# Performance work log

Hardware: AMD Instinct MI355X
Metric: run time of the kernel (lower is better)

Reference implementation:

```python
import jax, jax.numpy as jnp
import numpy as np

EPS = 1e-5

def _bn(x, g, b, axes):
    # BatchNorm (training-mode batch statistics), channel axis = 1
    m = jnp.mean(x, axis=axes, keepdims=True)
    v = jnp.var(x, axis=axes, keepdims=True)
    sh = [1] * x.ndim
    sh[1] = -1
    return (x - m) * jax.lax.rsqrt(v + EPS) * g.reshape(sh) + b.reshape(sh)

def _gelu(x):
    return jax.nn.gelu(x, approximate=False)  # torch nn.GELU default (erf)

def _knn_idx(x, k):
    # x: (B, C, N). Negative squared pairwise distance, take k nearest.
    inner = jnp.einsum('bcn,bcm->bnm', x, x)
    sq = jnp.sum(x * x, axis=1)                       # (B, N)
    negd = 2.0 * inner - sq[:, :, None] - sq[:, None, :]
    _, idx = jax.lax.top_k(negd, k)                   # (B, N, k) int32
    return idx

def _graph_feature(x, k):
    # x: (B, C, N) -> (B, 2C, N, k): concat(neighbor - center, center)
    idx = _knn_idx(x, k)
    xt = jnp.transpose(x, (0, 2, 1))                  # (B, N, C)
    nbr = jax.vmap(lambda xb, ib: xb[ib])(xt, idx)    # (B, N, k, C) gather
    ctr = jnp.broadcast_to(xt[:, :, None, :], nbr.shape)
    f = jnp.concatenate([nbr - ctr, ctr], axis=-1)    # (B, N, k, 2C)
    return jnp.transpose(f, (0, 3, 1, 2))             # (B, 2C, N, k)

def _edge_block(x, W, g, b, k):
    # gather -> 1x1 conv -> BN -> GELU -> max over neighbors
    f = _graph_feature(x, k)
    h = jnp.einsum('oi,bink->bonk', W, f)
    h = _gelu(_bn(h, g, b, (0, 2, 3)))
    return jnp.max(h, axis=-1)                        # (B, O, N)


def setup_inputs() -> dict:
    key = jax.random.key(0)
    ks = jax.random.split(key, 16)
    B, C, N, k = 8, 3, 1024, 20
    c = 64
    def w(kk, o, i):
        return jax.random.normal(kk, (o, i), jnp.float32) * (1.0 / np.sqrt(i))
    inp = {
        'x': jax.random.normal(ks[0], (B, C, N), jnp.float32),
        'k': k,
        'W1': w(ks[1], c, 2 * C),            # (64, 6)
        'g1': jnp.ones((c,)), 'b1': jnp.zeros((c,)),
        'W2': w(ks[2], 2 * c, 2 * c),        # (128, 128)
        'g2': jnp.ones((2 * c,)), 'b2': jnp.zeros((2 * c,)),
        'W3': w(ks[3], 4 * c, 4 * c),        # (256, 256)
        'g3': jnp.ones((4 * c,)), 'b3': jnp.zeros((4 * c,)),
        'W4': w(ks[4], 8 * c, 8 * c),        # (512, 512)
        'g4': jnp.ones((8 * c,)), 'b4': jnp.zeros((8 * c,)),
        'W5': w(ks[5], 16 * c, 15 * c),      # (1024, 960) cat(64+128+256+512)
        'g5': jnp.ones((16 * c,)), 'b5': jnp.zeros((16 * c,)),
        'Wl1': w(ks[6], 8 * c, 32 * c),      # (512, 2048), bias=False
        'g6': jnp.ones((8 * c,)), 'b6': jnp.zeros((8 * c,)),
        'Wl2': w(ks[7], 256, 512), 'bl2': jnp.zeros((256,)),
        'g7': jnp.ones((256,)), 'b7': jnp.zeros((256,)),
        'Wl3': w(ks[8], 40, 256), 'bl3': jnp.zeros((40,)),
    }
    return inp


def reference(x, k, W1, g1, b1, W2, g2, b2, W3, g3, b3, W4, g4, b4,
              W5, g5, b5, Wl1, g6, b6, Wl2, bl2, g7, b7, Wl3, bl3):
    x1 = _edge_block(x,  W1, g1, b1, k)   # (B, 64,  N)
    x2 = _edge_block(x1, W2, g2, b2, k)   # (B, 128, N)
    x3 = _edge_block(x2, W3, g3, b3, k)   # (B, 256, N)
    x4 = _edge_block(x3, W4, g4, b4, k)   # (B, 512, N)
    xc = jnp.concatenate([x1, x2, x3, x4], axis=1)  # (B, 960, N)
    h = jnp.einsum('oi,bin->bon', W5, xc)           # (B, 1024, N)
    h = _gelu(_bn(h, g5, b5, (0, 2)))
    mx = jnp.max(h, axis=-1)
    av = jnp.mean(h, axis=-1)
    z = jnp.concatenate([mx, av], axis=1)           # (B, 2048)
    z = z @ Wl1.T                                   # (B, 512), no bias
    z = jax.nn.leaky_relu(_bn(z, g6, b6, (0,)), 0.2)
    z = z @ Wl2.T + bl2                             # (B, 256)
    z = jax.nn.leaky_relu(_bn(z, g7, b7, (0,)), 0.2)
    out = z @ Wl3.T + bl3                           # (B, 40)
    return out
```

## Files before the change

kernel.cpp:

```cpp
#include <hip/hip_runtime.h>
#include <math.h>

#define BB 8
#define NN 1024
#define KNN 20

typedef unsigned short u16;
typedef __bf16 bf16x8 __attribute__((ext_vector_type(8)));
typedef float floatx4 __attribute__((ext_vector_type(4)));

__device__ __forceinline__ float gelu_erf(float x) {
    return 0.5f * x * (1.0f + erff(x * 0.70710678118654752440f));
}

__device__ __forceinline__ u16 f2bf(float f) {
    unsigned int u = __float_as_uint(f);
    unsigned int r = (u + 0x7fffu + ((u >> 16) & 1u)) >> 16;
    return (u16)r;
}
__device__ __forceinline__ float bf2f(u16 h) {
    return __uint_as_float(((unsigned int)h) << 16);
}

#define STATS_BLK 32768
#define STATS_TOTAL (4 * STATS_BLK + 16384)
#define ZERO_TOTAL (STATS_TOTAL + 3 * 8192)

__global__ void k_transpose(const float* __restrict__ x, float* __restrict__ x0,
                            float* __restrict__ sz) {
    int t = blockIdx.x * 256 + threadIdx.x;
    for (int i = t; i < ZERO_TOTAL; i += BB * NN) sz[i] = 0.f;
    if (t >= BB * NN) return;
    int b = t / NN, n = t % NN;
    #pragma unroll
    for (int c = 0; c < 3; ++c) x0[(size_t)t * 3 + c] = x[((size_t)b * 3 + c) * NN + n];
}

#define SEG2 16384
#define SEG3 81920
#define SEG4 344064
#define SEGT 1327104
__global__ void k_prep_w(const float* __restrict__ W2, const float* __restrict__ W3,
                         const float* __restrict__ W4, const float* __restrict__ W5,
                         u16* __restrict__ wh, u16* __restrict__ wl) {
    int t = blockIdx.x * 256 + threadIdx.x;
    if (t >= SEGT) return;
    float v;
    if (t < SEG2) {
        int row = t >> 6, c = t & 63;
        v = (row < 128) ? W2[row * 128 + c]
                        : W2[(row - 128) * 128 + 64 + c] - W2[(row - 128) * 128 + c];
    } else if (t < SEG3) {
        int i = t - SEG2;
        int row = i >> 7, c = i & 127;
        v = (row < 256) ? W3[row * 256 + c]
                        : W3[(row - 256) * 256 + 128 + c] - W3[(row - 256) * 256 + c];
    } else if (t < SEG4) {
        int i = t - SEG3;
        int row = i >> 8, c = i & 255;
        v = (row < 512) ? W4[row * 512 + c]
                        : W4[(row - 512) * 512 + 256 + c] - W4[(row - 512) * 512 + c];
    } else {
        int i = t - SEG4;
        int row = i / 960, c = i % 960;
        v = W5[row * 960 + c];
    }
    u16 h = f2bf(v);
    wh[t] = h;
    wl[t] = f2bf(v - bf2f(h));
}

__global__ void k_negd(const float* __restrict__ X, int SA, int Kc, float* __restrict__ out) {
    int bz = blockIdx.z;
    const float* Xb = X + (size_t)bz * NN * SA;
    float* Cout = out + (size_t)bz * NN * NN;
    int m0 = blockIdx.y * 128, n0 = blockIdx.x * 128;
    __shared__ float As[16][132];
    __shared__ float Bs[16][132];
    __shared__ float sqA[128];
    __shared__ float sqB[128];
    int t = threadIdx.x;
    int tx = t & 15, ty = t >> 4;
    int r = t >> 1, kb = (t & 1) * 8;
    float acc[2][2][4][4] = {};
    float sqa = 0.f, sqb = 0.f;
    for (int k0 = 0; k0 < Kc; k0 += 16) {
        const float* srcA = Xb + (size_t)(m0 + r) * SA + k0 + kb;
        const float* srcB = Xb + (size_t)(n0 + r) * SA + k0 + kb;
        #pragma unroll
        for (int i = 0; i < 8; ++i) {
            float va = (k0 + kb + i < Kc) ? srcA[i] : 0.f;
            float vb = (k0 + kb + i < Kc) ? srcB[i] : 0.f;
            As[kb + i][r] = va;
            Bs[kb + i][r] = vb;
            sqa = fmaf(va, va, sqa);
            sqb = fmaf(vb, vb, sqb);
        }
        __syncthreads();
        #pragma unroll
        for (int kk = 0; kk < 16; ++kk) {
            float4 a0 = *(const float4*)&As[kk][ty * 4];
            float4 a1 = *(const float4*)&As[kk][64 + ty * 4];
            float4 b0 = *(const float4*)&Bs[kk][tx * 4];
            float4 b1 = *(const float4*)&Bs[kk][64 + tx * 4];
            float av[2][4] = {{a0.x, a0.y, a0.z, a0.w}, {a1.x, a1.y, a1.z, a1.w}};
            float bv[2][4] = {{b0.x, b0.y, b0.z, b0.w}, {b1.x, b1.y, b1.z, b1.w}};
            #pragma unroll
            for (int hm = 0; hm < 2; ++hm)
                #pragma unroll
                for (int hn = 0; hn < 2; ++hn)
                    #pragma unroll
                    for (int i = 0; i < 4; ++i)
                        #pragma unroll
                        for (int j = 0; j < 4; ++j)
                            acc[hm][hn][i][j] = fmaf(av[hm][i], bv[hn][j], acc[hm][hn][i][j]);
        }
        __syncthreads();
    }
    sqa += __shfl_xor(sqa, 1);
    sqb += __shfl_xor(sqb, 1);
    if ((t & 1) == 0) { sqA[r] = sqa; sqB[r] = sqb; }
    __syncthreads();
    #pragma unroll
    for (int hm = 0; hm < 2; ++hm)
        #pragma unroll
        for (int i = 0; i < 4; ++i) {
            int lrow = hm * 64 + ty * 4 + i;
            float sm = sqA[lrow];
            float* crow = Cout + (size_t)(m0 + lrow) * NN + n0;
            #pragma unroll
            for (int hn = 0; hn < 2; ++hn) {
                float4 sn = *(const float4*)&sqB[hn * 64 + tx * 4];
                float4 v;
                v.x = 2.f * acc[hm][hn][i][0] - sm - sn.x;
                v.y = 2.f * acc[hm][hn][i][1] - sm - sn.y;
                v.z = 2.f * acc[hm][hn][i][2] - sm - sn.z;
                v.w = 2.f * acc[hm][hn][i][3] - sm - sn.w;
                *(float4*)&crow[hn * 64 + tx * 4] = v;
            }
        }
}

__global__ __launch_bounds__(256) void k_mfma_comb(
    const u16* __restrict__ Ah, const u16* __restrict__ Al,
    const u16* __restrict__ Wh, const u16* __restrict__ Wl,
    const float* __restrict__ sqg,
    float* __restrict__ negdOut, float* __restrict__ uwOut,
    int K, int ldUw) {
    const int lda = 960;
    int bx = blockIdx.x, by = blockIdx.y;
    bool gram = (by < 8);
    int m0, n0, rowBase;
    const u16 *pBh, *pBl;
    size_t ldb;
    float* pC;
    if (gram) {
        int b = bx & 7;
        n0 = (bx >> 3) * 128;
        m0 = by * 128;
        rowBase = b * NN;
        pBh = Ah; pBl = Al; ldb = lda;
        pC = negdOut + (size_t)b * NN * NN;
    } else {
        m0 = bx * 128;
        n0 = (by - 8) * 128;
        rowBase = 0;
        pBh = Wh; pBl = Wl; ldb = K;
        pC = uwOut;
    }
    __shared__ u16 sAh[4 * 1024];
    __shared__ u16 sAl[4 * 1024];
    __shared__ u16 sBh[4 * 1024];
    __shared__ u16 sBl[4 * 1024];
    __shared__ float sqA[128];
    __shared__ float sqB[128];
    int t = threadIdx.x;
    int w = t >> 6, lane = t & 63;
    int wm = (w & 1) * 64, wn = (w >> 1) * 64;
    int q = lane >> 4, lm = lane & 15;
    int r = t >> 1, cb = (t & 1) * 16;
    int q0 = (t & 1) * 2;
    if (gram) {
        if (t < 128) sqA[t] = sqg[rowBase + m0 + t];
        else if (t < 256) sqB[t - 128] = sqg[rowBase + n0 + (t - 128)];
    }
    floatx4 acc[4][4];
    #pragma unroll
    for (int i = 0; i < 4; ++i)
        #pragma unroll
        for (int j = 0; j < 4; ++j) {
            floatx4 z = {0.f, 0.f, 0.f, 0.f};
            acc[i][j] = z;
        }
    for (int k0 = 0; k0 < K; k0 += 32) {
        {
            size_t oa = (size_t)(rowBase + m0 + r) * lda + k0 + cb;
            size_t ob = gram ? (size_t)(rowBase + n0 + r) * lda + k0 + cb
                             : (size_t)(n0 + r) * ldb + k0 + cb;
            float4 ah0 = *(const float4*)&Ah[oa];
            float4 ah1 = *(const float4*)&Ah[oa + 8];
            float4 al0 = *(const float4*)&Al[oa];
            float4 al1 = *(const float4*)&Al[oa + 8];
            float4 bh0 = *(const float4*)&pBh[ob];
            float4 bh1 = *(const float4*)&pBh[ob + 8];
            float4 bl0 = *(const float4*)&pBl[ob];
            float4 bl1 = *(const float4*)&pBl[ob + 8];
            *(float4*)&sAh[q0 * 1024 + r * 8] = ah0;
            *(float4*)&sAh[(q0 + 1) * 1024 + r * 8] = ah1;
            *(float4*)&sAl[q0 * 1024 + r * 8] = al0;
            *(float4*)&sAl[(q0 + 1) * 1024 + r * 8] = al1;
            *(float4*)&sBh[q0 * 1024 + r * 8] = bh0;
            *(float4*)&sBh[(q0 + 1) * 1024 + r * 8] = bh1;
            *(float4*)&sBl[q0 * 1024 + r * 8] = bl0;
            *(float4*)&sBl[(q0 + 1) * 1024 + r * 8] = bl1;
        }
        __syncthreads();
        bf16x8 ah[4], al[4], bh[4], bl[4];
        #pragma unroll
        for (int i = 0; i < 4; ++i) {
            ah[i] = *(const bf16x8*)&sAh[q * 1024 + (wm + i * 16 + lm) * 8];
            al[i] = *(const bf16x8*)&sAl[q * 1024 + (wm + i * 16 + lm) * 8];
        }
        #pragma unroll
        for (int j = 0; j < 4; ++j) {
            bh[j] = *(const bf16x8*)&sBh[q * 1024 + (wn + j * 16 + lm) * 8];
            bl[j] = *(const bf16x8*)&sBl[q * 1024 + (wn + j * 16 + lm) * 8];
        }
        #pragma unroll
        for (int i = 0; i < 4; ++i)
            #pragma unroll
            for (int j = 0; j < 4; ++j) {
                acc[i][j] = __builtin_amdgcn_mfma_f32_16x16x32_bf16(ah[i], bh[j], acc[i][j], 0, 0, 0);
                acc[i][j] = __builtin_amdgcn_mfma_f32_16x16x32_bf16(ah[i], bl[j], acc[i][j], 0, 0, 0);
                acc[i][j] = __builtin_amdgcn_mfma_f32_16x16x32_bf16(al[i], bh[j], acc[i][j], 0, 0, 0);
            }
        __syncthreads();
    }
    if (gram) {
        #pragma unroll
        for (int i = 0; i < 4; ++i)
            #pragma unroll
            for (int j = 0; j < 4; ++j) {
                int coll = wn + j * 16 + lm;
                float sn = sqB[coll];
                #pragma unroll
                for (int rr = 0; rr < 4; ++rr) {
                    int rowl = wm + i * 16 + q * 4 + rr;
                    pC[(size_t)(m0 + rowl) * NN + n0 + coll] =
                        2.f * acc[i][j][rr] - sqA[rowl] - sn;
                }
            }
    } else {
        #pragma unroll
        for (int i = 0; i < 4; ++i) {
            int rowb = m0 + wm + i * 16 + q * 4;
            #pragma unroll
            for (int j = 0; j < 4; ++j) {
                int col = n0 + wn + j * 16 + lm;
                #pragma unroll
                for (int rr = 0; rr < 4; ++rr)
                    pC[(size_t)(rowb + rr) * ldUw + col] = acc[i][j][rr];
            }
        }
    }
}

__global__ __launch_bounds__(256) void k_mfma16(
    const u16* __restrict__ Ah, const u16* __restrict__ Al, int lda,
    const u16* __restrict__ Bh, const u16* __restrict__ Bl, int ldb,
    float* __restrict__ Cout, int ldc, int K) {
    int m0 = blockIdx.y * 128, n0 = blockIdx.x * 128;
    __shared__ u16 sAh[4 * 1024];
    __shared__ u16 sAl[4 * 1024];
    __shared__ u16 sBh[4 * 1024];
    __shared__ u16 sBl[4 * 1024];
    int t = threadIdx.x;
    int w = t >> 6, lane = t & 63;
    int wm = (w & 1) * 64, wn = (w >> 1) * 64;
    int q = lane >> 4, lm = lane & 15;
    int r = t >> 1, cb = (t & 1) * 16;
    int q0 = (t & 1) * 2;
    floatx4 acc[4][4];
    #pragma unroll
    for (int i = 0; i < 4; ++i)
        #pragma unroll
        for (int j = 0; j < 4; ++j) {
            floatx4 z = {0.f, 0.f, 0.f, 0.f};
            acc[i][j] = z;
        }
    for (int k0 = 0; k0 < K; k0 += 32) {
        {
            size_t oa = (size_t)(m0 + r) * lda + k0 + cb;
            size_t ob = (size_t)(n0 + r) * ldb + k0 + cb;
            float4 ah0 = *(const float4*)&Ah[oa];
            float4 ah1 = *(const float4*)&Ah[oa + 8];
            float4 al0 = *(const float4*)&Al[oa];
            float4 al1 = *(const float4*)&Al[oa + 8];
            float4 bh0 = *(const float4*)&Bh[ob];
            float4 bh1 = *(const float4*)&Bh[ob + 8];
            float4 bl0 = *(const float4*)&Bl[ob];
            float4 bl1 = *(const float4*)&Bl[ob + 8];
            *(float4*)&sAh[q0 * 1024 + r * 8] = ah0;
            *(float4*)&sAh[(q0 + 1) * 1024 + r * 8] = ah1;
            *(float4*)&sAl[q0 * 1024 + r * 8] = al0;
            *(float4*)&sAl[(q0 + 1) * 1024 + r * 8] = al1;
            *(float4*)&sBh[q0 * 1024 + r * 8] = bh0;
            *(float4*)&sBh[(q0 + 1) * 1024 + r * 8] = bh1;
            *(float4*)&sBl[q0 * 1024 + r * 8] = bl0;
            *(float4*)&sBl[(q0 + 1) * 1024 + r * 8] = bl1;
        }
        __syncthreads();
        bf16x8 ah[4], al[4], bh[4], bl[4];
        #pragma unroll
        for (int i = 0; i < 4; ++i) {
            ah[i] = *(const bf16x8*)&sAh[q * 1024 + (wm + i * 16 + lm) * 8];
            al[i] = *(const bf16x8*)&sAl[q * 1024 + (wm + i * 16 + lm) * 8];
        }
        #pragma unroll
        for (int j = 0; j < 4; ++j) {
            bh[j] = *(const bf16x8*)&sBh[q * 1024 + (wn + j * 16 + lm) * 8];
            bl[j] = *(const bf16x8*)&sBl[q * 1024 + (wn + j * 16 + lm) * 8];
        }
        #pragma unroll
        for (int i = 0; i < 4; ++i)
            #pragma unroll
            for (int j = 0; j < 4; ++j) {
                acc[i][j] = __builtin_amdgcn_mfma_f32_16x16x32_bf16(ah[i], bh[j], acc[i][j], 0, 0, 0);
                acc[i][j] = __builtin_amdgcn_mfma_f32_16x16x32_bf16(ah[i], bl[j], acc[i][j], 0, 0, 0);
                acc[i][j] = __builtin_amdgcn_mfma_f32_16x16x32_bf16(al[i], bh[j], acc[i][j], 0, 0, 0);
            }
        __syncthreads();
    }
    #pragma unroll
    for (int i = 0; i < 4; ++i) {
        int rowb = m0 + wm + i * 16 + q * 4;
        #pragma unroll
        for (int j = 0; j < 4; ++j) {
            int col = n0 + wn + j * 16 + lm;
            #pragma unroll
            for (int rr = 0; rr < 4; ++rr)
                Cout[(size_t)(rowb + rr) * ldc + col] = acc[i][j][rr];
        }
    }
}

__global__ void k_topk(const float* __restrict__ negd, int* __restrict__ idxout) {
    int wv = threadIdx.x >> 6, lane = threadIdx.x & 63;
    int bx = blockIdx.x;
    int b = bx & 7, rg = bx >> 3;
    int rowA = b * NN + rg * 8 + wv * 2;
    int rowB = rowA + 1;
    const float* dA = negd + (size_t)rowA * NN;
    const float* dB = negd + (size_t)rowB * NN;
    float va[16], vb[16];
    #pragma unroll
    for (int j = 0; j < 16; ++j) {
        va[j] = dA[j * 64 + lane];
        vb[j] = dB[j * 64 + lane];
    }
    float lva = va[0], lvb = vb[0];
    int lca = lane, lcb = lane;
    #pragma unroll
    for (int j = 1; j < 16; ++j) {
        int c = j * 64 + lane;
        if (va[j] > lva) { lva = va[j]; lca = c; }
        if (vb[j] > lvb) { lvb = vb[j]; lcb = c; }
    }
    for (int it = 0; it < KNN; ++it) {
        float ta = lva, tb = lvb;
        #pragma unroll
        for (int s = 32; s >= 1; s >>= 1) {
            float oa = __shfl_xor(ta, s);
            float ob = __shfl_xor(tb, s);
            ta = fmaxf(ta, oa);
            tb = fmaxf(tb, ob);
        }
        unsigned long long ma = __ballot(lva == ta);
        unsigned long long mb = __ballot(lvb == tb);
        int wa = 0x7fffffff, wb = 0x7fffffff;
        while (ma) {
            int l = __ffsll((unsigned long long)ma) - 1;
            int c = __shfl(lca, l);
            wa = min(wa, c);
            ma &= ma - 1;
        }
        while (mb) {
            int l = __ffsll((unsigned long long)mb) - 1;
            int c = __shfl(lcb, l);
            wb = min(wb, c);
            mb &= mb - 1;
        }
        if (lane == 0) {
            idxout[(size_t)rowA * KNN + it] = wa;
            idxout[(size_t)rowB * KNN + it] = wb;
        }
        if ((wa & 63) == lane) {
            int jd = wa >> 6;
            #pragma unroll
            for (int j = 0; j < 16; ++j)
                if (j == jd) va[j] = -INFINITY;
            lva = -INFINITY; lca = 0x7fffffff;
            #pragma unroll
            for (int j = 0; j < 16; ++j) {
                int c = j * 64 + lane;
                if (va[j] > lva) { lva = va[j]; lca = c; }
            }
        }
        if ((wb & 63) == lane) {
            int jd = wb >> 6;
            #pragma unroll
            for (int j = 0; j < 16; ++j)
                if (j == jd) vb[j] = -INFINITY;
            lvb = -INFINITY; lcb = 0x7fffffff;
            #pragma unroll
            for (int j = 0; j < 16; ++j) {
                int c = j * 64 + lane;
                if (vb[j] > lvb) { lvb = vb[j]; lcb = c; }
            }
        }
    }
}

__global__ void k_uw1(const float* __restrict__ x0, const float* __restrict__ W1,
                      float* __restrict__ uw) {
    int t = blockIdx.x * 256 + threadIdx.x;
    if (t >= BB * NN * 128) return;
    int r = t >> 7, o = t & 127;
    float xv0 = x0[(size_t)r * 3], xv1 = x0[(size_t)r * 3 + 1], xv2 = x0[(size_t)r * 3 + 2];
    float acc;
    if (o < 64) {
        const float* wr = W1 + (size_t)o * 6;
        acc = wr[0] * xv0 + wr[1] * xv1 + wr[2] * xv2;
    } else {
        const float* wr = W1 + (size_t)(o - 64) * 6;
        acc = (wr[3] - wr[0]) * xv0 + (wr[4] - wr[1]) * xv1 + (wr[5] - wr[2]) * xv2;
    }
    uw[(size_t)t] = acc;
}

__global__ void k_gather4(const float* __restrict__ uw, const int* __restrict__ idx,
                          int O, int ctc, int R,
                          float* __restrict__ hmin, float* __restrict__ hmax,
                          float* __restrict__ s1, float* __restrict__ s2) {
    int t = threadIdx.x;
    int ct = t % ctc, rt = t / ctc;
    int rowsPer = (R * ctc) >> 8;
    int bx = blockIdx.x;
    int b = bx & 7, rg = bx >> 3;
    int row0 = b * NN + rg * R;
    int shard = bx & 15;
    int o4 = blockIdx.y * (ctc * 4) + ct * 4;
    __shared__ int sidx[16 * KNN];
    __shared__ float4 red1[256];
    __shared__ float4 red2[256];
    for (int i = t; i < R * KNN; i += 256) sidx[i] = idx[(size_t)row0 * KNN + i];
    __syncthreads();
    int twoO = 2 * O;
    const float* ubase = uw + (size_t)b * NN * twoO;
    float a1[4] = {0, 0, 0, 0}, a2[4] = {0, 0, 0, 0};
    for (int rr = rt * rowsPer; rr < (rt + 1) * rowsPer; ++rr) {
        int nrow = row0 + rr;
        float4 w4 = *(const float4*)(uw + (size_t)nrow * twoO + O + o4);
        float wv[4] = {w4.x, w4.y, w4.z, w4.w};
        float mn[4], mx[4];
        #pragma unroll
        for (int qq = 0; qq < 4; ++qq) { mn[qq] = INFINITY; mx[qq] = -INFINITY; }
        #pragma unroll 4
        for (int j = 0; j < KNN; ++j) {
            int m = sidx[rr * KNN + j];
            float4 u4 = *(const float4*)(ubase + (size_t)m * twoO + o4);
            float uv[4] = {u4.x, u4.y, u4.z, u4.w};
            #pragma unroll
            for (int qq = 0; qq < 4; ++qq) {
                float h = uv[qq] + wv[qq];
                mn[qq] = fminf(mn[qq], h);
                mx[qq] = fmaxf(mx[qq], h);
                a1[qq] += h;
                a2[qq] = fmaf(h, h, a2[qq]);
            }
        }
        *(float4*)&hmin[(size_t)nrow * O + o4] = make_float4(mn[0], mn[1], mn[2], mn[3]);
        *(float4*)&hmax[(size_t)nrow * O + o4] = make_float4(mx[0], mx[1], mx[2], mx[3]);
    }
    red1[t] = make_float4(a1[0], a1[1], a1[2], a1[3]);
    red2[t] = make_float4(a2[0], a2[1], a2[2], a2[3]);
    __syncthreads();
    if (rt == 0) {
        int rs = 256 / ctc;
        for (int rr = 1; rr < rs; ++rr) {
            float4 v1 = red1[ct + rr * ctc];
            float4 v2 = red2[ct + rr * ctc];
            a1[0] += v1.x; a1[1] += v1.y; a1[2] += v1.z; a1[3] += v1.w;
            a2[0] += v2.x; a2[1] += v2.y; a2[2] += v2.z; a2[3] += v2.w;
        }
        #pragma unroll
        for (int qq = 0; qq < 4; ++qq) {
            atomicAdd(&s1[shard * O + o4 + qq], a1[qq]);
            atomicAdd(&s2[shard * O + o4 + qq], a2[qq]);
        }
    }
}

__global__ void k_bnfin(const float* __restrict__ s1, const float* __restrict__ s2,
                        const float* __restrict__ g, const float* __restrict__ b,
                        float cnt_inv, int O, float* __restrict__ scale,
                        float* __restrict__ shift) {
    int o = blockIdx.x * 256 + threadIdx.x;
    if (o >= O) return;
    float a1 = 0.f, a2 = 0.f;
    #pragma unroll
    for (int s = 0; s < 16; ++s) {
        a1 += s1[s * O + o];
        a2 += s2[s * O + o];
    }
    float mean = a1 * cnt_inv;
    float var = a2 * cnt_inv - mean * mean;
    float sc = g[o] * rsqrtf(var + 1e-5f);
    scale[o] = sc;
    shift[o] = b[o] - mean * sc;
}

__global__ void k_apply(const float* __restrict__ hmin, const float* __restrict__ hmax,
                        const float* __restrict__ scale, const float* __restrict__ shiftv,
                        int O, int shift,
                        u16* __restrict__ outh, u16* __restrict__ outl, int coloff,
                        float* __restrict__ sqout) {
    int gidx = blockIdx.x * 256 + threadIdx.x;
    int row = gidx >> shift;
    int o4 = (gidx & ((1 << shift) - 1)) * 4;
    ushort4 vh, vl;
    float sq = 0.f;
    float vals[4];
    #pragma unroll
    for (int qq = 0; qq < 4; ++qq) {
        int o = o4 + qq;
        float sc = scale[o], sh = shiftv[o];
        float va = gelu_erf(fmaf(sc, hmax[(size_t)row * O + o], sh));
        float vb = gelu_erf(fmaf(sc, hmin[(size_t)row * O + o], sh));
        vals[qq] = fmaxf(va, vb);
        sq = fmaf(vals[qq], vals[qq], sq);
    }
    vh.x = f2bf(vals[0]); vl.x = f2bf(vals[0] - bf2f(vh.x));
    vh.y = f2bf(vals[1]); vl.y = f2bf(vals[1] - bf2f(vh.y));
    vh.z = f2bf(vals[2]); vl.z = f2bf(vals[2] - bf2f(vh.z));
    vh.w = f2bf(vals[3]); vl.w = f2bf(vals[3] - bf2f(vh.w));
    *(ushort4*)&outh[(size_t)row * 960 + coloff + o4] = vh;
    *(ushort4*)&outl[(size_t)row * 960 + coloff + o4] = vl;
    if (sqout) {
        int gsz = 1 << shift;
        if (gsz > 64) gsz = 64;
        #pragma unroll
        for (int s = 1; s < 64; s <<= 1) {
            if (s < gsz) sq += __shfl_xor(sq, s);
        }
        if ((threadIdx.x & (gsz - 1)) == 0) atomicAdd(&sqout[row], sq);
    }
}

__global__ void k_colstats(const float* __restrict__ A, float* __restrict__ s1,
                           float* __restrict__ s2) {
    int o = blockIdx.x * 256 + threadIdx.x;
    int r0 = blockIdx.y * 64;
    int shard = blockIdx.y & 7;
    float a1 = 0.f, a2 = 0.f;
    for (int r = 0; r < 64; ++r) {
        float v = A[(size_t)(r0 + r) * 1024 + o];
        a1 += v;
        a2 = fmaf(v, v, a2);
    }
    atomicAdd(&s1[shard * 1024 + o], a1);
    atomicAdd(&s2[shard * 1024 + o], a2);
}

__global__ void k_apply5(const float* __restrict__ h5, const float* __restrict__ s1,
                         const float* __restrict__ s2, const float* __restrict__ g,
                         const float* __restrict__ b, float* __restrict__ pmax,
                         float* __restrict__ psum) {
    int o = blockIdx.x * 256 + threadIdx.x;
    int ch = blockIdx.y;
    int bb = blockIdx.z;
    float a1 = 0.f, a2 = 0.f;
    #pragma unroll
    for (int s = 0; s < 8; ++s) {
        a1 += s1[s * 1024 + o];
        a2 += s2[s * 1024 + o];
    }
    float mean = a1 * (1.0f / (BB * NN));
    float var = a2 * (1.0f / (BB * NN)) - mean * mean;
    float sc = g[o] * rsqrtf(var + 1e-5f);
    float sh = b[o] - mean * sc;
    int n0 = ch * (NN / 16);
    float mx = -INFINITY, sm = 0.f;
    for (int n = n0; n < n0 + NN / 16; ++n) {
        float v = gelu_erf(fmaf(sc, h5[((size_t)bb * NN + n) * 1024 + o], sh));
        mx = fmaxf(mx, v);
        sm += v;
    }
    pmax[((size_t)ch * BB + bb) * 1024 + o] = mx;
    psum[((size_t)ch * BB + bb) * 1024 + o] = sm;
}

__global__ void k_zfin(const float* __restrict__ pmax, const float* __restrict__ psum,
                       float* __restrict__ z) {
    int o = blockIdx.x * 256 + threadIdx.x;
    int bb = blockIdx.y;
    float mx = -INFINITY, sm = 0.f;
    for (int ch = 0; ch < 16; ++ch) {
        mx = fmaxf(mx, pmax[((size_t)ch * BB + bb) * 1024 + o]);
        sm += psum[((size_t)ch * BB + bb) * 1024 + o];
    }
    z[(size_t)bb * 2048 + o] = mx;
    z[(size_t)bb * 2048 + 1024 + o] = sm * (1.0f / NN);
}

template <int DOBN>
__global__ void k_fc(const float* __restrict__ Z, int Kc, const float* __restrict__ W,
                     const float* __restrict__ bias, const float* __restrict__ g,
                     const float* __restrict__ b, float* __restrict__ out, int Oc) {
    int o = blockIdx.x;
    int lane = threadIdx.x;
    float acc[BB];
    #pragma unroll
    for (int q = 0; q < BB; ++q) acc[q] = 0.f;
    const float* wrow = W + (size_t)o * Kc;
    for (int i = lane; i < Kc; i += 64) {
        float wv = wrow[i];
        #pragma unroll
        for (int q = 0; q < BB; ++q) acc[q] = fmaf(Z[(size_t)q * Kc + i], wv, acc[q]);
    }
    #pragma unroll
    for (int s = 32; s > 0; s >>= 1) {
        #pragma unroll
        for (int q = 0; q < BB; ++q) acc[q] += __shfl_xor(acc[q], s);
    }
    if (lane == 0) {
        float bv = bias ? bias[o] : 0.f;
        float v[BB];
        #pragma unroll
        for (int q = 0; q < BB; ++q) v[q] = acc[q] + bv;
        if (DOBN) {
            float m = 0.f;
            #pragma unroll
            for (int q = 0; q < BB; ++q) m += v[q];
            m *= (1.0f / BB);
            float var = 0.f;
            #pragma unroll
            for (int q = 0; q < BB; ++q) { float d = v[q] - m; var = fmaf(d, d, var); }
            var *= (1.0f / BB);
            float sc = g[o] * rsqrtf(var + 1e-5f);
            #pragma unroll
            for (int q = 0; q < BB; ++q) {
                float y = fmaf(v[q] - m, sc, b[o]);
                v[q] = (y >= 0.f) ? y : 0.2f * y;
            }
        }
        #pragma unroll
        for (int q = 0; q < BB; ++q) out[(size_t)q * Oc + o] = v[q];
    }
}

extern "C" void kernel_launch(void* const* d_in, const int* in_sizes, int n_in,
                              void* d_out, int out_size, void* d_ws, size_t ws_size,
                              hipStream_t stream) {
    (void)in_sizes; (void)n_in; (void)out_size; (void)ws_size;
    const float* x   = (const float*)d_in[0];
    const float* W1  = (const float*)d_in[2];
    const float* g1  = (const float*)d_in[3];
    const float* b1  = (const float*)d_in[4];
    const float* W2  = (const float*)d_in[5];
    const float* g2  = (const float*)d_in[6];
    const float* b2  = (const float*)d_in[7];
    const float* W3  = (const float*)d_in[8];
    const float* g3  = (const float*)d_in[9];
    const float* b3  = (const float*)d_in[10];
    const float* W4  = (const float*)d_in[11];
    const float* g4  = (const float*)d_in[12];
    const float* b4  = (const float*)d_in[13];
    const float* W5  = (const float*)d_in[14];
    const float* g5  = (const float*)d_in[15];
    const float* b5  = (const float*)d_in[16];
    const float* Wl1 = (const float*)d_in[17];
    const float* g6  = (const float*)d_in[18];
    const float* b6  = (const float*)d_in[19];
    const float* Wl2 = (const float*)d_in[20];
    const float* bl2 = (const float*)d_in[21];
    const float* g7  = (const float*)d_in[22];
    const float* b7  = (const float*)d_in[23];
    const float* Wl3 = (const float*)d_in[24];
    const float* bl3 = (const float*)d_in[25];

    char* p = (char*)d_ws;
    auto carve = [&](size_t nbytes) {
        char* q = p;
        p += (nbytes + 255) & ~(size_t)255;
        return (void*)q;
    };
    float* x0   = (float*)carve((size_t)BB * NN * 3 * 4);
    float* negd = (float*)carve((size_t)BB * NN * NN * 4);
    int*   idx  = (int*)carve((size_t)BB * NN * KNN * 4);
    float* uw   = (float*)carve((size_t)BB * NN * 1024 * 4);
    u16*   xch  = (u16*)carve((size_t)BB * NN * 960 * 2);
    u16*   xcl  = (u16*)carve((size_t)BB * NN * 960 * 2);
    u16*   wh   = (u16*)carve((size_t)SEGT * 2);
    u16*   wl   = (u16*)carve((size_t)SEGT * 2);
    float* sz   = (float*)carve((size_t)ZERO_TOTAL * 4);
    float* sqb  = sz + STATS_TOTAL;
    float* scale= (float*)carve(1024 * 4);
    float* shiftv = (float*)carve(1024 * 4);
    float* pmax = (float*)carve((size_t)16 * BB * 1024 * 4);
    float* psum = (float*)carve((size_t)16 * BB * 1024 * 4);
    float* z    = (float*)carve((size_t)BB * 2048 * 4);
    float* z1   = (float*)carve((size_t)BB * 512 * 4);
    float* z2   = (float*)carve((size_t)BB * 256 * 4);
    float* hmin = negd;
    float* hmax = negd + (size_t)BB * NN * 512;

    k_transpose<<<dim3(32), dim3(256), 0, stream>>>(x, x0, sz);
    k_prep_w<<<dim3(SEGT / 256), dim3(256), 0, stream>>>(W2, W3, W4, W5, wh, wl);

    const float* gs[4] = {g1, g2, g3, g4};
    const float* bs[4] = {b1, b2, b3, b4};
    int Cs[4] = {3, 64, 128, 256};
    int Os[4] = {64, 128, 256, 512};
    int coloff[4] = {0, 64, 192, 448};
    int ioff[4]   = {0, 0, 64, 192};
    int woff[4] = {0, 0, SEG2, SEG3};
    int ctcs[4] = {16, 32, 64, 64};
    int gys[4]  = {1, 1, 1, 2};
    int Rs[4]   = {16, 8, 8, 8};
    int shifts[4] = {4, 5, 6, 7};
    float cnt_inv = 1.0f / ((float)BB * NN * KNN);

    for (int blk = 0; blk < 4; ++blk) {
        int C = Cs[blk], O = Os[blk];
        if (blk == 0) {
            k_negd<<<dim3(8, 8, BB), dim3(256), 0, stream>>>(x0, 3, 3, negd);
            k_topk<<<dim3(BB * NN / 8), dim3(256), 0, stream>>>(negd, idx);
            k_uw1<<<dim3(BB * NN * 128 / 256), dim3(256), 0, stream>>>(x0, W1, uw);
        } else {
            k_mfma_comb<<<dim3(64, 8 + 2 * O / 128), dim3(256), 0, stream>>>(
                xch + ioff[blk], xcl + ioff[blk],
                wh + woff[blk], wl + woff[blk],
                sqb + (blk - 1) * 8192, negd, uw, C, 2 * O);
            k_topk<<<dim3(BB * NN / 8), dim3(256), 0, stream>>>(negd, idx);
        }
        float* s1 = sz + blk * STATS_BLK;
        float* s2 = s1 + 16 * O;
        k_gather4<<<dim3(8 * (NN / Rs[blk]), gys[blk]), dim3(256), 0, stream>>>(
            uw, idx, O, ctcs[blk], Rs[blk], hmin, hmax, s1, s2);
        k_bnfin<<<dim3((O + 255) / 256), dim3(256), 0, stream>>>(
            s1, s2, gs[blk], bs[blk], cnt_inv, O, scale, shiftv);
        k_apply<<<dim3(BB * NN * (O / 4) / 256), dim3(256), 0, stream>>>(
            hmin, hmax, scale, shiftv, O, shifts[blk],
            xch, xcl, coloff[blk], (blk < 3) ? (sqb + blk * 8192) : (float*)nullptr);
    }

    k_mfma16<<<dim3(8, 64), dim3(256), 0, stream>>>(
        xch, xcl, 960, wh + SEG4, wl + SEG4, 960, uw, 1024, 960);
    float* s15 = sz + 4 * STATS_BLK;
    float* s25 = s15 + 8 * 1024;
    k_colstats<<<dim3(4, BB * NN / 64), dim3(256), 0, stream>>>(uw, s15, s25);
    k_apply5<<<dim3(4, 16, BB), dim3(256), 0, stream>>>(uw, s15, s25, g5, b5, pmax, psum);
    k_zfin<<<dim3(4, BB), dim3(256), 0, stream>>>(pmax, psum, z);

    k_fc<1><<<dim3(512), dim3(64), 0, stream>>>(z, 2048, Wl1, (const float*)nullptr, g6, b6, z1, 512);
    k_fc<1><<<dim3(256), dim3(64), 0, stream>>>(z1, 512, Wl2, bl2, g7, b7, z2, 256);
    k_fc<0><<<dim3(40), dim3(64), 0, stream>>>(z2, 256, Wl3, bl3, (const float*)nullptr,
                                               (const float*)nullptr, (float*)d_out, 40);
}
```

Measured before the change: 617.8 us.

## Exploit Gram matrix symmetry: compute upper-triangle tiles and mirror-store transpose

The combined MFMA kernel now uses a 1D grid: the first 288 blocks cover only the upper-triangular 128x128 tiles of each batch's pairwise-distance matrix (36 per batch), and off-diagonal tiles also write their transposed values. The remaining blocks handle the feature-weight GEMM, with tile coordinates computed from the linear index. This roughly halves the Gram-matrix MFMA work, at the cost of extra strided float4 stores for the mirrored tiles and a small loop to decode the triangular index. Exact symmetry holds because the 3-term bf16 split product is symmetric in its operands.

```diff
diff --git a/kernel.cpp b/kernel.cpp
--- a/kernel.cpp
+++ b/kernel.cpp
@@ -148,22 +148,30 @@
     float* __restrict__ negdOut, float* __restrict__ uwOut,
     int K, int ldUw) {
     const int lda = 960;
-    int bx = blockIdx.x, by = blockIdx.y;
-    bool gram = (by < 8);
+    int u = blockIdx.x;
+    bool gram = (u < 288);
     int m0, n0, rowBase;
+    bool mirror = false;
     const u16 *pBh, *pBl;
     size_t ldb;
     float* pC;
     if (gram) {
-        int b = bx & 7;
-        n0 = (bx >> 3) * 128;
-        m0 = by * 128;
+        int b = u & 7;
+        int p = u >> 3;
+        int ti = 0, rem = p;
+        while (rem >= 8 - ti) { rem -= 8 - ti; ++ti; }
+        int tj = ti + rem;
+        m0 = ti * 128;
+        n0 = tj * 128;
+        mirror = (ti != tj);
         rowBase = b * NN;
         pBh = Ah; pBl = Al; ldb = lda;
         pC = negdOut + (size_t)b * NN * NN;
     } else {
-        m0 = bx * 128;
-        n0 = (by - 8) * 128;
+        int v = u - 288;
+        int nT = ldUw >> 7;
+        m0 = (v / nT) * 128;
+        n0 = (v % nT) * 128;
         rowBase = 0;
         pBh = Wh; pBl = Wl; ldb = K;
         pC = uwOut;
@@ -243,11 +251,16 @@
             for (int j = 0; j < 4; ++j) {
                 int coll = wn + j * 16 + lm;
                 float sn = sqB[coll];
+                float vals[4];
                 #pragma unroll
                 for (int rr = 0; rr < 4; ++rr) {
                     int rowl = wm + i * 16 + q * 4 + rr;
-                    pC[(size_t)(m0 + rowl) * NN + n0 + coll] =
-                        2.f * acc[i][j][rr] - sqA[rowl] - sn;
+                    vals[rr] = 2.f * acc[i][j][rr] - sqA[rowl] - sn;
+                    pC[(size_t)(m0 + rowl) * NN + n0 + coll] = vals[rr];
+                }
+                if (mirror) {
+                    float4 v4 = make_float4(vals[0], vals[1], vals[2], vals[3]);
+                    *(float4*)&pC[(size_t)(n0 + coll) * NN + m0 + wm + i * 16 + q * 4] = v4;
                 }
             }
     } else {
@@ -738,7 +751,7 @@
             k_topk<<<dim3(BB * NN / 8), dim3(256), 0, stream>>>(negd, idx);
             k_uw1<<<dim3(BB * NN * 128 / 256), dim3(256), 0, stream>>>(x0, W1, uw);
         } else {
-            k_mfma_comb<<<dim3(64, 8 + 2 * O / 128), dim3(256), 0, stream>>>(
+            k_mfma_comb<<<dim3(288 + 64 * (2 * O / 128)), dim3(256), 0, stream>>>(
                 xch + ioff[blk], xcl + ioff[blk],
                 wh + woff[blk], wl + woff[blk],
                 sqb + (blk - 1) * 8192, negd, uw, C, 2 * O);
```

Result: no change. 625.5 us (+1.2%).
